# Optimization experiments

Hardware: AMD Instinct MI355X
Metric: run time of the kernel (lower is better)

The kernel has to match this reference:

```python
import jax, jax.numpy as jnp
import numpy as np

N_LEVELS = 16
FEAT = 2
LOG2_T = 19
T = 1 << LOG2_T
PER_LEVEL_SCALE = 1.5
BASE_RES = 16
SCALE = 1.0
N_FREQ = 3
HASH_PRIME = np.uint32(2654435761)


def _level_params(level):
    # tcnn HashGrid: scale = 2^(level*log2(pls)) * base_res - 1; res = ceil(scale)+1
    scale = float(2.0 ** (level * np.log2(PER_LEVEL_SCALE)) * BASE_RES - 1.0)
    res = int(np.ceil(scale)) + 1
    return scale, res


def hash_encode(xy, tables):
    # xy: [N,2] in [0,1]; tables: [N_LEVELS, T, FEAT]
    outs = []
    for l in range(N_LEVELS):
        scale, res = _level_params(l)
        pos = xy * scale + 0.5
        pos_f = jnp.floor(pos)
        frac = pos - pos_f              # [N,2]
        pi = pos_f.astype(jnp.int32)    # [N,2]
        dense = (res * res) <= T

        def idx(ix, iy):
            if dense:
                return ix + iy * res
            h = ix.astype(jnp.uint32) ^ (iy.astype(jnp.uint32) * HASH_PRIME)
            return (h % np.uint32(T)).astype(jnp.int32)

        ix, iy = pi[:, 0], pi[:, 1]
        tbl = tables[l]
        f00 = tbl[idx(ix, iy)]
        f10 = tbl[idx(ix + 1, iy)]
        f01 = tbl[idx(ix, iy + 1)]
        f11 = tbl[idx(ix + 1, iy + 1)]
        wx = frac[:, 0:1]
        wy = frac[:, 1:2]
        outs.append((f00 * (1 - wx) + f10 * wx) * (1 - wy)
                    + (f01 * (1 - wx) + f11 * wx) * wy)
    return jnp.concatenate(outs, axis=-1)  # [N, 32]


def prior_net(xy, Wp1, Wp2, Wp3):
    # tcnn Frequency encoding (3 freqs, sin+cos per dim) + bias-free sigmoid MLP
    freqs = (2.0 ** jnp.arange(N_FREQ, dtype=jnp.float32)) * jnp.pi
    ang = xy[:, :, None] * freqs  # [N,2,3]
    enc = jnp.concatenate([jnp.sin(ang), jnp.cos(ang)], axis=-1).reshape(xy.shape[0], -1)  # [N,12]
    h = jax.nn.sigmoid(enc @ Wp1)
    h = jax.nn.sigmoid(h @ Wp2)
    return h @ Wp3  # [N,1]


def setup_inputs() -> dict:
    key = jax.random.key(0)
    ks = jax.random.split(key, 7)
    N = 2_000_000
    inputs = jax.random.normal(ks[0], (N, 3), dtype=jnp.float32)
    # tcnn-style small init for hash table entries
    hash_tables = jax.random.uniform(ks[1], (N_LEVELS, T, FEAT), dtype=jnp.float32,
                                     minval=-1e-4, maxval=1e-4)
    in_dim = N_LEVELS * FEAT  # 32
    W_tiny = jax.random.normal(ks[2], (in_dim, 65), dtype=jnp.float32) / np.sqrt(in_dim)
    b_tiny = jnp.zeros((65,), dtype=jnp.float32)
    Wp1 = jax.random.normal(ks[3], (2 * 2 * N_FREQ, 64), dtype=jnp.float32) / np.sqrt(12.0)
    Wp2 = jax.random.normal(ks[4], (64, 64), dtype=jnp.float32) / 8.0
    Wp3 = jax.random.normal(ks[5], (64, 1), dtype=jnp.float32) / 8.0
    return {"inputs": inputs, "hash_tables": hash_tables, "W_tiny": W_tiny,
            "b_tiny": b_tiny, "Wp1": Wp1, "Wp2": Wp2, "Wp3": Wp3}


def reference(inputs, hash_tables, W_tiny, b_tiny, Wp1, Wp2, Wp3):
    # forward_core(inputs, 0, output_height=False, delta=True, gradient=False)
    prior_z = jax.lax.stop_gradient(prior_net(inputs[:, :2], Wp1, Wp2, Wp3))  # detached
    z_vals = inputs[:, 2:]           # taken BEFORE scaling, as in torch code
    xin = inputs * SCALE
    feat = hash_encode(xin[:, :2] / 30.0 + 0.5, hash_tables)
    x = feat @ W_tiny + b_tiny       # [N,65]
    return jnp.concatenate([z_vals - x[:, :1] / SCALE - prior_z, x[:, 1:]], axis=-1)
```

## Files before the change

kernel.cpp:

```cpp
#include <hip/hip_runtime.h>

#define TSZ (1u << 19)
#define HPRIME 2654435761u

typedef short bf16x8 __attribute__((ext_vector_type(8)));
typedef float f32x4 __attribute__((ext_vector_type(4)));

__device__ __forceinline__ float sigmoidf(float x) {
    return 1.0f / (1.0f + __expf(-x));
}

__device__ __forceinline__ unsigned short f2b(float f) {
    union { float f; unsigned u; } v; v.f = f;
    return (unsigned short)((v.u + 0x7FFFu + ((v.u >> 16) & 1u)) >> 16);
}

__device__ __forceinline__ unsigned f2b_pack(float a, float b) {
    union { float f; unsigned u; } x, y; x.f = a; y.f = b;
    unsigned ra = (x.u + 0x7FFFu + ((x.u >> 16) & 1u)) >> 16;
    unsigned rb = (y.u + 0x7FFFu + ((y.u >> 16) & 1u)) & 0xFFFF0000u;
    return ra | rb;
}

__global__ void repack_frags(const float* __restrict__ Wp2,
                             const float* __restrict__ Wt,
                             unsigned short* __restrict__ wp2F,
                             unsigned short* __restrict__ wtF) {
    int t = blockIdx.x * blockDim.x + threadIdx.x;
    if (t < 4096) {
        int j = t & 7, lane = (t >> 3) & 63, f = t >> 9;
        int ks = f >> 2, nt = f & 3;
        int k = ks * 32 + (lane >> 4) * 8 + j;
        int n = nt * 16 + (lane & 15);
        wp2F[t] = f2b(Wp2[k * 64 + n]);
    }
    if (t < 2048) {
        int j = t & 7, lane = (t >> 3) & 63, nt = t >> 9;
        int k = (lane >> 4) * 8 + j;
        int n = nt * 16 + (lane & 15);
        wtF[t] = f2b(Wt[k * 65 + 1 + n]);
    }
}

__global__ __launch_bounds__(256)
void sdf_main(const float* __restrict__ in,
              const float* __restrict__ tables,
              const float* __restrict__ Wp1,
              const float* __restrict__ Wp3,
              const float* __restrict__ bt,
              const float* __restrict__ Wt,
              const unsigned short* __restrict__ wp2F,
              const unsigned short* __restrict__ wtF,
              float* __restrict__ out, int N)
{
    __shared__ unsigned short Abuf[4 * 64 * 72];
    __shared__ float sOut[64 * 65];
    __shared__ float sPrior[256];

    const int tid = threadIdx.x;
    const int wave = tid >> 6, lane = tid & 63;
    const int quad = lane >> 4, col = lane & 15;
    const long long n0 = (long long)blockIdx.x * 256;
    const int n = (int)n0 + tid;
    const int nc = n < N ? n : N - 1;

    const float px = in[nc * 3 + 0];
    const float py = in[nc * 3 + 1];
    const float pz = in[nc * 3 + 2];

    const float PIF = 3.14159274101257324e+00f;
    float e[12];
    e[0] = __sinf(px * PIF); e[1]  = __sinf(px * (2.0f * PIF)); e[2]  = __sinf(px * (4.0f * PIF));
    e[3] = __cosf(px * PIF); e[4]  = __cosf(px * (2.0f * PIF)); e[5]  = __cosf(px * (4.0f * PIF));
    e[6] = __sinf(py * PIF); e[7]  = __sinf(py * (2.0f * PIF)); e[8]  = __sinf(py * (4.0f * PIF));
    e[9] = __cosf(py * PIF); e[10] = __cosf(py * (2.0f * PIF)); e[11] = __cosf(py * (4.0f * PIF));

    unsigned short* myA = Abuf + wave * 64 * 72 + lane * 72;
#pragma unroll
    for (int j4 = 0; j4 < 64; j4 += 4) {
        float s0 = 0.f, s1 = 0.f, s2 = 0.f, s3 = 0.f;
#pragma unroll
        for (int k = 0; k < 12; k++) {
            const float4 w = *(const float4*)(Wp1 + k * 64 + j4);
            s0 += e[k] * w.x; s1 += e[k] * w.y; s2 += e[k] * w.z; s3 += e[k] * w.w;
        }
        uint2 pk;
        pk.x = f2b_pack(sigmoidf(s0), sigmoidf(s1));
        pk.y = f2b_pack(sigmoidf(s2), sigmoidf(s3));
        *reinterpret_cast<uint2*>(myA + j4) = pk;
    }
    __syncthreads();

    bf16x8 bfr[8];
#pragma unroll
    for (int f = 0; f < 8; f++)
        bfr[f] = *reinterpret_cast<const bf16x8*>(wp2F + (f * 64 + lane) * 8);
    float w3[4];
#pragma unroll
    for (int nt = 0; nt < 4; nt++) w3[nt] = Wp3[nt * 16 + col];

#pragma unroll
    for (int mt = 0; mt < 4; mt++) {
        const unsigned short* ar = Abuf + wave * 4608 + (mt * 16 + col) * 72;
        const bf16x8 a0 = *reinterpret_cast<const bf16x8*>(ar + quad * 8);
        const bf16x8 a1 = *reinterpret_cast<const bf16x8*>(ar + 32 + quad * 8);
        float pp[4] = {0.f, 0.f, 0.f, 0.f};
#pragma unroll
        for (int nt = 0; nt < 4; nt++) {
            f32x4 acc = {0.f, 0.f, 0.f, 0.f};
            acc = __builtin_amdgcn_mfma_f32_16x16x32_bf16(a0, bfr[nt], acc, 0, 0, 0);
            acc = __builtin_amdgcn_mfma_f32_16x16x32_bf16(a1, bfr[4 + nt], acc, 0, 0, 0);
#pragma unroll
            for (int r = 0; r < 4; r++)
                pp[r] += w3[nt] * sigmoidf(acc[r]);
        }
#pragma unroll
        for (int r = 0; r < 4; r++) {
            pp[r] += __shfl_xor(pp[r], 1, 64);
            pp[r] += __shfl_xor(pp[r], 2, 64);
            pp[r] += __shfl_xor(pp[r], 4, 64);
            pp[r] += __shfl_xor(pp[r], 8, 64);
            if (col == r) sPrior[wave * 64 + mt * 16 + quad * 4 + r] = pp[r];
        }
    }

    const float scl[16] = {15.f, 23.f, 35.f, 53.f, 80.f, 120.5f, 181.25f, 272.375f,
                           409.0625f, 614.09375f, 921.640625f, 1382.9609375f,
                           2074.94140625f, 3112.912109375f, 4669.8681640625f,
                           7005.30224609375f};
    const int ress[10] = {16, 24, 36, 54, 81, 122, 183, 274, 411, 616};
    const float cx = __fadd_rn(__fdiv_rn(px, 30.0f), 0.5f);
    const float cy = __fadd_rn(__fdiv_rn(py, 30.0f), 0.5f);

    unsigned short* myF = Abuf + wave * 4608 + lane * 40;
    float x0 = bt[0];
    unsigned pk[4];
#pragma unroll
    for (int l = 0; l < 16; l++) {
        const float sc = scl[l];
        const float posx = __fadd_rn(__fmul_rn(cx, sc), 0.5f);
        const float posy = __fadd_rn(__fmul_rn(cy, sc), 0.5f);
        const float fx = floorf(posx), fy = floorf(posy);
        const float wx = __fsub_rn(posx, fx), wy = __fsub_rn(posy, fy);
        const int ix = (int)fx, iy = (int)fy;
        const float* tbl = tables + (size_t)l * (size_t)(TSZ * 2);
        int i00, i10, i01, i11;
        if (l < 10) {
            const int r = ress[l];
            i00 = ix + iy * r; i10 = i00 + 1; i01 = i00 + r; i11 = i01 + 1;
        } else {
            const unsigned ux = (unsigned)ix, uy = (unsigned)iy;
            const unsigned hy0 = uy * HPRIME, hy1 = (uy + 1u) * HPRIME;
            i00 = (int)((ux ^ hy0) & (TSZ - 1u));
            i10 = (int)(((ux + 1u) ^ hy0) & (TSZ - 1u));
            i01 = (int)((ux ^ hy1) & (TSZ - 1u));
            i11 = (int)(((ux + 1u) ^ hy1) & (TSZ - 1u));
        }
        const float2 q00 = *(const float2*)(tbl + 2 * i00);
        const float2 q10 = *(const float2*)(tbl + 2 * i10);
        const float2 q01 = *(const float2*)(tbl + 2 * i01);
        const float2 q11 = *(const float2*)(tbl + 2 * i11);
        const float omx = 1.0f - wx, omy = 1.0f - wy;
        const float f0 = (q00.x * omx + q10.x * wx) * omy + (q01.x * omx + q11.x * wx) * wy;
        const float f1 = (q00.y * omx + q10.y * wx) * omy + (q01.y * omx + q11.y * wx) * wy;
        x0 += f0 * Wt[(2 * l) * 65] + f1 * Wt[(2 * l + 1) * 65];
        pk[l & 3] = f2b_pack(f0, f1);
        if ((l & 3) == 3) {
            uint4 v; v.x = pk[0]; v.y = pk[1]; v.z = pk[2]; v.w = pk[3];
            *reinterpret_cast<uint4*>(myF + (l - 3) * 2) = v;
        }
    }
    __syncthreads();

    const float priorMe = sPrior[wave * 64 + lane];

    for (int q = 0; q < 4; q++) {
        if (wave == q) {
            bf16x8 fa[4];
#pragma unroll
            for (int mt = 0; mt < 4; mt++)
                fa[mt] = *reinterpret_cast<const bf16x8*>(
                    Abuf + wave * 4608 + (mt * 16 + col) * 40 + quad * 8);
#pragma unroll
            for (int nt = 0; nt < 4; nt++) {
                const bf16x8 wb = *reinterpret_cast<const bf16x8*>(wtF + (nt * 64 + lane) * 8);
                const float bb = bt[1 + nt * 16 + col];
#pragma unroll
                for (int mt = 0; mt < 4; mt++) {
                    f32x4 acc = {0.f, 0.f, 0.f, 0.f};
                    acc = __builtin_amdgcn_mfma_f32_16x16x32_bf16(fa[mt], wb, acc, 0, 0, 0);
#pragma unroll
                    for (int r = 0; r < 4; r++)
                        sOut[(mt * 16 + quad * 4 + r) * 65 + 1 + nt * 16 + col] = acc[r] + bb;
                }
            }
            sOut[lane * 65] = pz - x0 - priorMe;
        }
        __syncthreads();
        const long long rbase = n0 + (long long)q * 64;
        float* op = out + (size_t)rbase * 65;
#pragma unroll
        for (int i = 0; i < 17; i++) {
            const int t = tid + i * 256;
            if (t < 4160 && rbase + t / 65 < N) op[t] = sOut[t];
        }
        __syncthreads();
    }
}

extern "C" void kernel_launch(void* const* d_in, const int* in_sizes, int n_in,
                              void* d_out, int out_size, void* d_ws, size_t ws_size,
                              hipStream_t stream) {
    const float* inputs = (const float*)d_in[0];
    const float* tables = (const float*)d_in[1];
    const float* W_tiny = (const float*)d_in[2];
    const float* b_tiny = (const float*)d_in[3];
    const float* Wp1    = (const float*)d_in[4];
    const float* Wp2    = (const float*)d_in[5];
    const float* Wp3    = (const float*)d_in[6];
    float* out = (float*)d_out;
    unsigned short* wp2F = (unsigned short*)d_ws;
    unsigned short* wtF  = wp2F + 4096;

    const int N = in_sizes[0] / 3;

    hipLaunchKernelGGL(repack_frags, dim3(16), dim3(256), 0, stream,
                       Wp2, W_tiny, wp2F, wtF);

    const int grid = (N + 255) / 256;
    hipLaunchKernelGGL(sdf_main, dim3(grid), dim3(256), 0, stream,
                       inputs, tables, Wp1, Wp3, b_tiny, W_tiny, wp2F, wtF, out, N);
}
```

Baseline: 1.016 ms.

## Write tiny-MLP outputs directly from MFMA registers and drop block-wide staging

Removes the shared-memory output staging buffer and the serialized per-wave loop with block barriers. Each wave now computes its own 64-row output tile and stores it directly to global memory, with a bounds-checked path for the tail. Other barriers that only protected per-wave data are dropped, and a min-blocks-per-CU launch bound is added. The aim is to cut barrier stalls and shared-memory traffic and let all waves work at once. The cost is less coalesced global stores: short 64-byte row segments instead of one contiguous block copy.

```diff
diff --git a/kernel.cpp b/kernel.cpp
--- a/kernel.cpp
+++ b/kernel.cpp
@@ -42,7 +42,7 @@
     }
 }
 
-__global__ __launch_bounds__(256)
+__global__ __launch_bounds__(256, 4)
 void sdf_main(const float* __restrict__ in,
               const float* __restrict__ tables,
               const float* __restrict__ Wp1,
@@ -54,7 +54,6 @@
               float* __restrict__ out, int N)
 {
     __shared__ unsigned short Abuf[4 * 64 * 72];
-    __shared__ float sOut[64 * 65];
     __shared__ float sPrior[256];
 
     const int tid = threadIdx.x;
@@ -89,7 +88,6 @@
         pk.y = f2b_pack(sigmoidf(s2), sigmoidf(s3));
         *reinterpret_cast<uint2*>(myA + j4) = pk;
     }
-    __syncthreads();
 
     bf16x8 bfr[8];
 #pragma unroll
@@ -170,41 +168,46 @@
             *reinterpret_cast<uint4*>(myF + (l - 3) * 2) = v;
         }
     }
-    __syncthreads();
 
     const float priorMe = sPrior[wave * 64 + lane];
 
-    for (int q = 0; q < 4; q++) {
-        if (wave == q) {
-            bf16x8 fa[4];
-#pragma unroll
-            for (int mt = 0; mt < 4; mt++)
-                fa[mt] = *reinterpret_cast<const bf16x8*>(
-                    Abuf + wave * 4608 + (mt * 16 + col) * 40 + quad * 8);
+    {
+        bf16x8 fa[4];
+#pragma unroll
+        for (int mt = 0; mt < 4; mt++)
+            fa[mt] = *reinterpret_cast<const bf16x8*>(
+                Abuf + wave * 4608 + (mt * 16 + col) * 40 + quad * 8);
+        bf16x8 wb[4];
+        float bb[4];
+#pragma unroll
+        for (int nt = 0; nt < 4; nt++) {
+            wb[nt] = *reinterpret_cast<const bf16x8*>(wtF + (nt * 64 + lane) * 8);
+            bb[nt] = bt[1 + nt * 16 + col];
+        }
+        const long long wbase = n0 + (long long)wave * 64;
+        float* op = out + (size_t)wbase * 65;
+        const bool full = (wbase + 64 <= (long long)N);
+#pragma unroll
+        for (int mt = 0; mt < 4; mt++) {
 #pragma unroll
             for (int nt = 0; nt < 4; nt++) {
-                const bf16x8 wb = *reinterpret_cast<const bf16x8*>(wtF + (nt * 64 + lane) * 8);
-                const float bb = bt[1 + nt * 16 + col];
-#pragma unroll
-                for (int mt = 0; mt < 4; mt++) {
-                    f32x4 acc = {0.f, 0.f, 0.f, 0.f};
-                    acc = __builtin_amdgcn_mfma_f32_16x16x32_bf16(fa[mt], wb, acc, 0, 0, 0);
+                f32x4 acc = {0.f, 0.f, 0.f, 0.f};
+                acc = __builtin_amdgcn_mfma_f32_16x16x32_bf16(fa[mt], wb[nt], acc, 0, 0, 0);
+                if (full) {
 #pragma unroll
                     for (int r = 0; r < 4; r++)
-                        sOut[(mt * 16 + quad * 4 + r) * 65 + 1 + nt * 16 + col] = acc[r] + bb;
+                        op[(mt * 16 + quad * 4 + r) * 65 + 1 + nt * 16 + col] = acc[r] + bb[nt];
+                } else {
+#pragma unroll
+                    for (int r = 0; r < 4; r++) {
+                        const int row = mt * 16 + quad * 4 + r;
+                        if (wbase + row < (long long)N)
+                            op[(size_t)row * 65 + 1 + nt * 16 + col] = acc[r] + bb[nt];
+                    }
                 }
             }
-            sOut[lane * 65] = pz - x0 - priorMe;
-        }
-        __syncthreads();
-        const long long rbase = n0 + (long long)q * 64;
-        float* op = out + (size_t)rbase * 65;
-#pragma unroll
-        for (int i = 0; i < 17; i++) {
-            const int t = tid + i * 256;
-            if (t < 4160 && rbase + t / 65 < N) op[t] = sOut[t];
-        }
-        __syncthreads();
+        }
+        if (n < N) out[(size_t)n * 65] = pz - x0 - priorMe;
     }
 }
 
```

Result: faster. 919.3 us (-9.5%).
